# Performance work log

Hardware: AMD Instinct MI355X
Metric: run time of the kernel (lower is better)

## Reference

```python
import jax, jax.numpy as jnp
import numpy as np
from jax import lax

GN_EPS = 1e-5


def _conv2d(x, w, b, pad):
    # x: (N, C, H, W), w: (O, I, kh, kw)
    y = lax.conv_general_dilated(x, w, window_strides=(1, 1),
                                 padding=[(pad, pad), (pad, pad)],
                                 dimension_numbers=('NCHW', 'OIHW', 'NCHW'))
    return y + b[None, :, None, None]


def _eca(x, eca_w, eca_b):
    # x: (N, C, H, W) -> channel attention (N, C, 1, 1)
    y = jnp.mean(x, axis=(2, 3))[:, None, :]  # (N, 1, C) : GAP then treat C as length
    y = lax.conv_general_dilated(y, eca_w, window_strides=(1,),
                                 padding=[(1, 1)],
                                 dimension_numbers=('NCH', 'OIH', 'NCH'))
    y = jax.nn.sigmoid(y + eca_b[None, :, None])  # (N, 1, C)
    return y[:, 0, :, None, None]  # (N, C, 1, 1)


def _group_norm_per_channel(x, gn_w, gn_b):
    # num_groups == num_channels: normalize each channel over (H, W)
    mean = jnp.mean(x, axis=(2, 3), keepdims=True)
    var = jnp.var(x, axis=(2, 3), keepdims=True)
    xhat = (x - mean) * lax.rsqrt(var + GN_EPS)
    return xhat * gn_w[None, :, None, None] + gn_b[None, :, None, None]


def setup_inputs() -> dict:
    key = jax.random.key(0)
    ks = jax.random.split(key, 8)
    b, c, h, w = 16, 512, 64, 64
    cg = c // 32  # 16
    s = 1.0 / np.sqrt(cg)
    return {
        'x': jax.random.normal(ks[0], (b, c, h, w), jnp.float32),
        'conv1x1_w': jax.random.normal(ks[1], (cg, cg, 1, 1), jnp.float32) * s,
        'conv1x1_b': jnp.zeros((cg,), jnp.float32),
        'conv3x3_w': jax.random.normal(ks[2], (cg, cg, 3, 3), jnp.float32) * (s / 3),
        'conv3x3_b': jnp.zeros((cg,), jnp.float32),
        'conv5x5_w': jax.random.normal(ks[3], (cg, cg, 5, 5), jnp.float32) * (s / 5),
        'conv5x5_b': jnp.zeros((cg,), jnp.float32),
        'gn_w': jnp.ones((cg,), jnp.float32),
        'gn_b': jnp.zeros((cg,), jnp.float32),
        'eca_w': jax.random.normal(ks[4], (1, 1, 3), jnp.float32) * 0.5,
        'eca_b': jnp.zeros((1,), jnp.float32),
        'groups': 32,
    }


def reference(x, conv1x1_w, conv1x1_b, conv3x3_w, conv3x3_b,
              conv5x5_w, conv5x5_b, gn_w, gn_b, eca_w, eca_b, groups):
    b, c, h, w = x.shape
    cg = c // groups
    bg = b * groups
    group_x = x.reshape(bg, cg, h, w)

    # coordinate attention branch
    x_h = jnp.mean(group_x, axis=3, keepdims=True)            # (bg, cg, h, 1)
    x_w = jnp.mean(group_x, axis=2, keepdims=True)            # (bg, cg, 1, w)
    x_w_t = jnp.transpose(x_w, (0, 1, 3, 2))                  # (bg, cg, w, 1)
    hw = _conv2d(jnp.concatenate([x_h, x_w_t], axis=2), conv1x1_w, conv1x1_b, 0)
    x_h2, x_w2 = hw[:, :, :h, :], hw[:, :, h:, :]             # (bg,cg,h,1), (bg,cg,w,1)
    gated = group_x * jax.nn.sigmoid(x_h2) * jax.nn.sigmoid(jnp.transpose(x_w2, (0, 1, 3, 2)))
    x1 = _group_norm_per_channel(gated, gn_w, gn_b)

    # parallel conv branches
    x2 = _conv2d(group_x, conv3x3_w, conv3x3_b, 1)
    x3 = _conv2d(group_x, conv5x5_w, conv5x5_b, 2)

    # shared ECA channel attention over the three branches
    ca = _eca(x1, eca_w, eca_b) + _eca(x2, eca_w, eca_b) + _eca(x3, eca_w, eca_b)
    group_x = group_x * ca

    # cross-scale softmax-bmm interactions
    def chan_softmax(v):
        # (bg, cg, h, w) -> softmax over channel means -> (bg, 1, cg)
        return jax.nn.softmax(jnp.mean(v, axis=(2, 3)), axis=-1)[:, None, :]

    x11, x21, x31 = chan_softmax(x1), chan_softmax(x2), chan_softmax(x3)
    f1 = x1.reshape(bg, cg, h * w)
    f2 = x2.reshape(bg, cg, h * w)
    f3 = x3.reshape(bg, cg, h * w)

    weights = (jnp.matmul(x11, f2) + jnp.matmul(x11, f3)
               + jnp.matmul(x21, f1) + jnp.matmul(x21, f3)
               + jnp.matmul(x31, f1) + jnp.matmul(x31, f2))  # (bg, 1, h*w)
    weights = jax.nn.sigmoid(weights.reshape(bg, 1, h, w))

    return (group_x * weights).reshape(b, c, h, w)
```

## Files before the change

### kernel.cpp

```cpp
#include <hip/hip_runtime.h>

typedef unsigned int u32;

#define CG   16
#define HWN  4096
#define LSTR 68

__device__ __forceinline__ float sigm(float x) { return 1.0f / (1.0f + __expf(-x)); }

__global__ __launch_bounds__(512, 4) void ema_kernel(
    const float* __restrict__ x,
    const float* __restrict__ w1, const float* __restrict__ b1,
    const float* __restrict__ w3, const float* __restrict__ b3,
    const float* __restrict__ w5, const float* __restrict__ b5,
    const float* __restrict__ gnw, const float* __restrict__ gnb,
    const float* __restrict__ ew, const float* __restrict__ eb,
    float* __restrict__ out)
{
  __shared__ __align__(16) float s_cb[2][68][LSTR];
  __shared__ __align__(16) float s_row[16][64];
  __shared__ __align__(16) float s_col[16][64];
  __shared__ __align__(16) float s_RS[16][25];
  __shared__ float s_p2[16][16], s_p3[16][16];
  __shared__ __align__(16) float s_sh[16][64];
  __shared__ __align__(16) float s_sw[16][64];
  __shared__ __align__(16) float s_W5[16][28];
  __shared__ float s_ca[16], s_A1[16], s_Cc[16];
  __shared__ float s_w1[256], s_b1[16], s_gnw[16], s_gnb[16], s_b3[16], s_b5[16], s_ecaw[3], s_ecab[1];
  __shared__ float s_m2[16], s_m3[16], s_sm1[16], s_sm2[16], s_sm3[16];
  __shared__ float s_a1[16], s_a2[16], s_a3[16], s_total[16];
  __shared__ float s_red[16][8][2];
  __shared__ float s_scal[2];

  const int g = blockIdx.x;
  const int t = threadIdx.x;
  const int wv = t >> 6;
  const int ln = t & 63;
  const float* px   = x   + (size_t)g * CG * HWN;
  float*       pout = out + (size_t)g * CG * HWN;

  {
    const int j4 = ln & 15;
    const int rr = ln >> 4;
    #pragma unroll 1
    for (int cc = 0; cc < 2; ++cc) {
      const int c = 2 * wv + cc;
      float rs[16];
      float cp0 = 0.f, cp1 = 0.f, cp2 = 0.f, cp3 = 0.f;
      #pragma unroll
      for (int j = 0; j < 16; ++j) {
        float4 v = *(const float4*)(px + c * HWN + (rr + 4 * j) * 64 + 4 * j4);
        rs[j] = v.x + v.y + v.z + v.w;
        cp0 += v.x; cp1 += v.y; cp2 += v.z; cp3 += v.w;
      }
      #pragma unroll
      for (int j = 0; j < 16; ++j) {
        float r = rs[j];
        r += __shfl_xor(r, 1); r += __shfl_xor(r, 2);
        r += __shfl_xor(r, 4); r += __shfl_xor(r, 8);
        if (j4 == 0) s_row[c][rr + 4 * j] = r;
      }
      cp0 += __shfl_xor(cp0, 16); cp0 += __shfl_xor(cp0, 32);
      cp1 += __shfl_xor(cp1, 16); cp1 += __shfl_xor(cp1, 32);
      cp2 += __shfl_xor(cp2, 16); cp2 += __shfl_xor(cp2, 32);
      cp3 += __shfl_xor(cp3, 16); cp3 += __shfl_xor(cp3, 32);
      if (rr == 0) *(float4*)&s_col[c][4 * j4] = make_float4(cp0, cp1, cp2, cp3);
    }
  }
  if (t < 256) s_w1[t] = w1[t];
  if (t < 16) {
    s_b1[t]  = b1[t];  s_gnw[t] = gnw[t]; s_gnb[t] = gnb[t];
    s_b3[t]  = b3[t];  s_b5[t]  = b5[t];
  }
  if (t < 3)  s_ecaw[t] = ew[t];
  if (t == 0) s_ecab[0] = eb[0];
  __syncthreads();

  if (t < 16) { float s = 0.f; for (int y = 0; y < 64; ++y) s += s_row[t][y]; s_total[t] = s; }
  __syncthreads();

  #pragma unroll
  for (int m = 0; m < 4; ++m) {
    int idx = t + 512 * m; int o = idx >> 7, pos = idx & 127;
    float acc = s_b1[o];
    const float inv64 = 1.0f / 64.0f;
    #pragma unroll
    for (int i = 0; i < 16; ++i) {
      float v = (pos < 64 ? s_row[i][pos] : s_col[i][pos - 64]) * inv64;
      acc += s_w1[o * 16 + i] * v;
    }
    float sg = sigm(acc);
    if (pos < 64) s_sh[o][pos] = sg; else s_sw[o][pos - 64] = sg;
  }
  #pragma unroll
  for (int m = 0; m < 5; ++m) { int idx = t + 512 * m; if (idx < 2312) ((float4*)s_cb)[idx] = make_float4(0.f, 0.f, 0.f, 0.f); }
  if (t < 400) {
    int i = t / 25, kk = t % 25;
    int dy = kk / 5 - 2, dx = kk % 5 - 2;
    int a  = dy > 0 ? dy : 0,   b  = 64 + (dy < 0 ? dy : 0);
    int cl = dx > 0 ? dx : 0,   d  = 64 + (dx < 0 ? dx : 0);
    float S = s_total[i];
    if (a > 0)  S -= s_row[i][0];
    if (a > 1)  S -= s_row[i][1];
    if (b < 64) S -= s_row[i][63];
    if (b < 63) S -= s_row[i][62];
    for (int x0 = 0; x0 < cl; ++x0) {
      float cv = s_col[i][x0];
      if (a > 0)  cv -= px[i * HWN + 0 * 64  + x0];
      if (a > 1)  cv -= px[i * HWN + 1 * 64  + x0];
      if (b < 64) cv -= px[i * HWN + 63 * 64 + x0];
      if (b < 63) cv -= px[i * HWN + 62 * 64 + x0];
      S -= cv;
    }
    for (int x0 = d; x0 < 64; ++x0) {
      float cv = s_col[i][x0];
      if (a > 0)  cv -= px[i * HWN + 0 * 64  + x0];
      if (a > 1)  cv -= px[i * HWN + 1 * 64  + x0];
      if (b < 64) cv -= px[i * HWN + 63 * 64 + x0];
      if (b < 63) cv -= px[i * HWN + 62 * 64 + x0];
      S -= cv;
    }
    s_RS[i][kk] = S;
  }
  __syncthreads();

  if (t < 256) {
    int o = t >> 4, i = t & 15;
    float p2 = 0.f, p3 = 0.f;
    const float* w3b = w3 + (o * 16 + i) * 9;
    const float* w5b = w5 + (o * 16 + i) * 25;
    #pragma unroll
    for (int ky = 0; ky < 3; ++ky)
      #pragma unroll
      for (int kx = 0; kx < 3; ++kx)
        p2 += w3b[ky * 3 + kx] * s_RS[i][(ky + 1) * 5 + (kx + 1)];
    #pragma unroll
    for (int kk = 0; kk < 25; ++kk) p3 += w5b[kk] * s_RS[i][kk];
    s_p2[o][i] = p2; s_p3[o][i] = p3;
  }
  __syncthreads();
  if (t < 16)      { float s = 0.f; for (int i = 0; i < 16; ++i) s += s_p2[t][i];      s_m2[t] = s_b3[t] + s * (1.0f/4096.0f); }
  else if (t < 32) { int o = t - 16; float s = 0.f; for (int i = 0; i < 16; ++i) s += s_p3[o][i]; s_m3[o] = s_b5[o] + s * (1.0f/4096.0f); }
  __syncthreads();

  if (t < 3) {
    const float* m = (t == 0) ? s_gnb : (t == 1) ? s_m2 : s_m3;
    float* dst     = (t == 0) ? s_sm1 : (t == 1) ? s_sm2 : s_sm3;
    float mx = m[0];
    for (int c = 1; c < 16; ++c) mx = fmaxf(mx, m[c]);
    float e[16], ssum = 0.f;
    for (int c = 0; c < 16; ++c) { e[c] = __expf(m[c] - mx); ssum += e[c]; }
    float r = 1.0f / ssum;
    for (int c = 0; c < 16; ++c) dst[c] = e[c] * r;
  }
  __syncthreads();

  if (t < 16) {
    int c = t;
    float casum = 0.f;
    #pragma unroll
    for (int v = 0; v < 3; ++v) {
      const float* m = (v == 0) ? s_gnb : (v == 1) ? s_m2 : s_m3;
      float acc = s_ecab[0] + s_ecaw[1] * m[c];
      if (c > 0)  acc += s_ecaw[0] * m[c - 1];
      if (c < 15) acc += s_ecaw[2] * m[c + 1];
      casum += sigm(acc);
    }
    s_ca[c] = casum;
    s_a1[c] = s_sm2[c] + s_sm3[c];
    s_a2[c] = s_sm1[c] + s_sm3[c];
    s_a3[c] = s_sm1[c] + s_sm2[c];
  }
  __syncthreads();

  #define STAGE(buf, c) {                                                \
    _Pragma("unroll")                                                    \
    for (int k = 0; k < 2; ++k) {                                        \
      int q = t + 512 * k;                                               \
      int rr = q >> 4, xc = (q & 15) * 4;                                \
      float4 v = *(const float4*)(px + (size_t)(c) * HWN + rr * 64 + xc);\
      float* d = &s_cb[buf][2 + rr][2 + xc];                             \
      *(float2*)d       = make_float2(v.x, v.y);                         \
      *(float2*)(d + 2) = make_float2(v.z, v.w);                         \
    }                                                                    \
  }

  if (t == 0) {
    float s = 0.f;
    for (int o = 0; o < 16; ++o) s += s_a2[o] * s_b3[o] + s_a3[o] * s_b5[o];
    s_scal[1] = s;
  }
  if (t < 448) {
    if (t < 400) {
      int i = t / 25, kk = t % 25, ky = kk / 5, kx = kk % 5;
      float acc = 0.f;
      #pragma unroll
      for (int o = 0; o < 16; ++o) acc += s_a3[o] * w5[((o * 16 + i) * 5 + ky) * 5 + kx];
      if (ky >= 1 && ky <= 3 && kx >= 1 && kx <= 3) {
        #pragma unroll
        for (int o = 0; o < 16; ++o) acc += s_a2[o] * w3[((o * 16 + i) * 3 + (ky - 1)) * 3 + (kx - 1)];
      }
      s_W5[i][kk] = acc;
    } else {
      int q = t - 400; s_W5[q / 3][25 + q % 3] = 0.f;
    }
  }
  STAGE(0, 0);
  __syncthreads();

  const int x0 = 4 * (t & 15);
  const int y0 = 2 * (t >> 4);

  float ws[8];
  #pragma unroll
  for (int i = 0; i < 8; ++i) ws[i] = 0.f;
  float gsv[2][8];

  #pragma unroll 1
  for (int c = 0; c < 16; ++c) {
    if (c < 15) STAGE((c + 1) & 1, c + 1);
    if (c >= 1 && t == 0) {
      float S = 0.f, Q = 0.f;
      #pragma unroll
      for (int w = 0; w < 8; ++w) { S += s_red[c-1][w][0]; Q += s_red[c-1][w][1]; }
      float mu  = S * (1.0f / 4096.0f);
      float var = Q * (1.0f / 4096.0f) - mu * mu;
      float inv = rsqrtf(var + 1e-5f);
      s_A1[c-1] = s_a1[c-1] * s_gnw[c-1] * inv;
      s_Cc[c-1] = s_a1[c-1] * (s_gnb[c-1] - mu * s_gnw[c-1] * inv);
    }
    if (c >= 2) {
      float a1v = s_A1[c-2];
      #pragma unroll
      for (int i = 0; i < 8; ++i) ws[i] += a1v * gsv[c & 1][i];
    }
    float Wk[28];
    #pragma unroll
    for (int i = 0; i < 7; ++i) *(float4*)&Wk[4 * i] = *(float4*)&s_W5[c][4 * i];
    float shv0 = s_sh[c][y0], shv1 = s_sh[c][y0 + 1];
    float swv[4];
    #pragma unroll
    for (int r = 0; r < 4; ++r) swv[r] = s_sw[c][x0 + r];
    const float* base = &s_cb[c & 1][0][0] + y0 * LSTR + x0;
    float gsl = 0.f, gql = 0.f;
    #pragma unroll
    for (int q = 0; q < 6; ++q) {
      const float* rp = base + q * LSTR;
      float4 A = *(const float4*)rp, B = *(const float4*)(rp + 4);
      float v[8] = {A.x, A.y, A.z, A.w, B.x, B.y, B.z, B.w};
      if (q == 2 || q == 3) {
        const float sh_ = (q == 2) ? shv0 : shv1;
        const int ri = q - 2;
        #pragma unroll
        for (int m = 0; m < 4; ++m) {
          float gg = v[m + 2] * sh_ * swv[m];
          gsl += gg; gql += gg * gg;
          gsv[c & 1][4 * ri + m] = gg;
        }
      }
      #pragma unroll
      for (int r = 0; r < 2; ++r) {
        const int kr = q - r;
        if (kr >= 0 && kr <= 4) {
          #pragma unroll
          for (int m = 0; m < 4; ++m) {
            float a = ws[4 * r + m];
            a += Wk[kr * 5 + 0] * v[m + 0];
            a += Wk[kr * 5 + 1] * v[m + 1];
            a += Wk[kr * 5 + 2] * v[m + 2];
            a += Wk[kr * 5 + 3] * v[m + 3];
            a += Wk[kr * 5 + 4] * v[m + 4];
            ws[4 * r + m] = a;
          }
        }
      }
    }
    gsl += __shfl_xor(gsl, 1);  gql += __shfl_xor(gql, 1);
    gsl += __shfl_xor(gsl, 2);  gql += __shfl_xor(gql, 2);
    gsl += __shfl_xor(gsl, 4);  gql += __shfl_xor(gql, 4);
    gsl += __shfl_xor(gsl, 8);  gql += __shfl_xor(gql, 8);
    gsl += __shfl_xor(gsl, 16); gql += __shfl_xor(gql, 16);
    gsl += __shfl_xor(gsl, 32); gql += __shfl_xor(gql, 32);
    if (ln == 0) { s_red[c][wv][0] = gsl; s_red[c][wv][1] = gql; }
    __syncthreads();
  }

  if (t == 0) {
    float S = 0.f, Q = 0.f;
    #pragma unroll
    for (int w = 0; w < 8; ++w) { S += s_red[15][w][0]; Q += s_red[15][w][1]; }
    float mu  = S * (1.0f / 4096.0f);
    float var = Q * (1.0f / 4096.0f) - mu * mu;
    float inv = rsqrtf(var + 1e-5f);
    s_A1[15] = s_a1[15] * s_gnw[15] * inv;
    s_Cc[15] = s_a1[15] * (s_gnb[15] - mu * s_gnw[15] * inv);
    float s = s_scal[1];
    for (int c = 0; c < 16; ++c) s += s_Cc[c];
    s_scal[0] = s;
  }
  __syncthreads();
  {
    const float a14 = s_A1[14], a15 = s_A1[15], Ct = s_scal[0];
    #pragma unroll
    for (int i = 0; i < 8; ++i)
      ws[i] = sigm(ws[i] + a14 * gsv[0][i] + a15 * gsv[1][i] + Ct);
  }

  #pragma unroll
  for (int c = 0; c < 16; ++c) {
    const float cav = s_ca[c];
    const float* xp = px   + c * HWN + y0 * 64 + x0;
    float*       op = pout + c * HWN + y0 * 64 + x0;
    float4 xa = *(const float4*)xp;
    float4 xb = *(const float4*)(xp + 64);
    float4 oa, ob;
    oa.x = xa.x * cav * ws[0]; oa.y = xa.y * cav * ws[1];
    oa.z = xa.z * cav * ws[2]; oa.w = xa.w * cav * ws[3];
    ob.x = xb.x * cav * ws[4]; ob.y = xb.y * cav * ws[5];
    ob.z = xb.z * cav * ws[6]; ob.w = xb.w * cav * ws[7];
    *(float4*)op        = oa;
    *(float4*)(op + 64) = ob;
  }
}

extern "C" void kernel_launch(void* const* d_in, const int* in_sizes, int n_in,
                              void* d_out, int out_size, void* d_ws, size_t ws_size,
                              hipStream_t stream) {
  const float* X  = (const float*)d_in[0];
  const float* W1 = (const float*)d_in[1];
  const float* B1 = (const float*)d_in[2];
  const float* W3 = (const float*)d_in[3];
  const float* B3 = (const float*)d_in[4];
  const float* W5 = (const float*)d_in[5];
  const float* B5 = (const float*)d_in[6];
  const float* GW = (const float*)d_in[7];
  const float* GB = (const float*)d_in[8];
  const float* EW = (const float*)d_in[9];
  const float* EB = (const float*)d_in[10];
  float* O = (float*)d_out;
  ema_kernel<<<dim3(512), dim3(512), 0, stream>>>(X, W1, B1, W3, B3, W5, B5, GW, GB, EW, EB, O);
}
```

Measured before the change: 345.1 us.

## Alias scratch arrays into conv staging buffer, split staging load/write, nontemporal stores

Reuses the second half of the double-buffered conv tile for the row/col sums, RS and partial-product scratch, cutting LDS per block, and raises the launch-bounds occupancy hint from 4 to 6 blocks per CU. Staging of the next channel is split into a global load issued at the top of the loop and an LDS write after the conv compute, so the load latency is hidden behind the arithmetic. Output stores become nontemporal. The split keeps extra live registers across the loop, which together with the tighter launch bound risks spills.

```diff
diff --git a/kernel.cpp b/kernel.cpp
--- a/kernel.cpp
+++ b/kernel.cpp
@@ -1,6 +1,7 @@
 #include <hip/hip_runtime.h>
 
 typedef unsigned int u32;
+typedef float f4v __attribute__((ext_vector_type(4)));
 
 #define CG   16
 #define HWN  4096
@@ -8,7 +9,7 @@
 
 __device__ __forceinline__ float sigm(float x) { return 1.0f / (1.0f + __expf(-x)); }
 
-__global__ __launch_bounds__(512, 4) void ema_kernel(
+__global__ __launch_bounds__(512, 6) void ema_kernel(
     const float* __restrict__ x,
     const float* __restrict__ w1, const float* __restrict__ b1,
     const float* __restrict__ w3, const float* __restrict__ b3,
@@ -18,10 +19,11 @@
     float* __restrict__ out)
 {
   __shared__ __align__(16) float s_cb[2][68][LSTR];
-  __shared__ __align__(16) float s_row[16][64];
-  __shared__ __align__(16) float s_col[16][64];
-  __shared__ __align__(16) float s_RS[16][25];
-  __shared__ float s_p2[16][16], s_p3[16][16];
+  float* const s_row = &s_cb[1][0][0];
+  float* const s_col = s_row + 1024;
+  float* const s_RS  = s_row + 2048;
+  float* const s_p2  = s_row + 2448;
+  float* const s_p3  = s_row + 2704;
   __shared__ __align__(16) float s_sh[16][64];
   __shared__ __align__(16) float s_sw[16][64];
   __shared__ __align__(16) float s_W5[16][28];
@@ -58,13 +60,13 @@
         float r = rs[j];
         r += __shfl_xor(r, 1); r += __shfl_xor(r, 2);
         r += __shfl_xor(r, 4); r += __shfl_xor(r, 8);
-        if (j4 == 0) s_row[c][rr + 4 * j] = r;
+        if (j4 == 0) s_row[c * 64 + rr + 4 * j] = r;
       }
       cp0 += __shfl_xor(cp0, 16); cp0 += __shfl_xor(cp0, 32);
       cp1 += __shfl_xor(cp1, 16); cp1 += __shfl_xor(cp1, 32);
       cp2 += __shfl_xor(cp2, 16); cp2 += __shfl_xor(cp2, 32);
       cp3 += __shfl_xor(cp3, 16); cp3 += __shfl_xor(cp3, 32);
-      if (rr == 0) *(float4*)&s_col[c][4 * j4] = make_float4(cp0, cp1, cp2, cp3);
+      if (rr == 0) *(float4*)&s_col[c * 64 + 4 * j4] = make_float4(cp0, cp1, cp2, cp3);
     }
   }
   if (t < 256) s_w1[t] = w1[t];
@@ -76,7 +78,7 @@
   if (t == 0) s_ecab[0] = eb[0];
   __syncthreads();
 
-  if (t < 16) { float s = 0.f; for (int y = 0; y < 64; ++y) s += s_row[t][y]; s_total[t] = s; }
+  if (t < 16) { float s = 0.f; for (int y = 0; y < 64; ++y) s += s_row[t * 64 + y]; s_total[t] = s; }
   __syncthreads();
 
   #pragma unroll
@@ -86,26 +88,26 @@
     const float inv64 = 1.0f / 64.0f;
     #pragma unroll
     for (int i = 0; i < 16; ++i) {
-      float v = (pos < 64 ? s_row[i][pos] : s_col[i][pos - 64]) * inv64;
+      float v = (pos < 64 ? s_row[i * 64 + pos] : s_col[i * 64 + pos - 64]) * inv64;
       acc += s_w1[o * 16 + i] * v;
     }
     float sg = sigm(acc);
     if (pos < 64) s_sh[o][pos] = sg; else s_sw[o][pos - 64] = sg;
   }
   #pragma unroll
-  for (int m = 0; m < 5; ++m) { int idx = t + 512 * m; if (idx < 2312) ((float4*)s_cb)[idx] = make_float4(0.f, 0.f, 0.f, 0.f); }
+  for (int m = 0; m < 3; ++m) { int idx = t + 512 * m; if (idx < 1156) ((float4*)&s_cb[0][0][0])[idx] = make_float4(0.f, 0.f, 0.f, 0.f); }
   if (t < 400) {
     int i = t / 25, kk = t % 25;
     int dy = kk / 5 - 2, dx = kk % 5 - 2;
     int a  = dy > 0 ? dy : 0,   b  = 64 + (dy < 0 ? dy : 0);
     int cl = dx > 0 ? dx : 0,   d  = 64 + (dx < 0 ? dx : 0);
     float S = s_total[i];
-    if (a > 0)  S -= s_row[i][0];
-    if (a > 1)  S -= s_row[i][1];
-    if (b < 64) S -= s_row[i][63];
-    if (b < 63) S -= s_row[i][62];
+    if (a > 0)  S -= s_row[i * 64 + 0];
+    if (a > 1)  S -= s_row[i * 64 + 1];
+    if (b < 64) S -= s_row[i * 64 + 63];
+    if (b < 63) S -= s_row[i * 64 + 62];
     for (int x0 = 0; x0 < cl; ++x0) {
-      float cv = s_col[i][x0];
+      float cv = s_col[i * 64 + x0];
       if (a > 0)  cv -= px[i * HWN + 0 * 64  + x0];
       if (a > 1)  cv -= px[i * HWN + 1 * 64  + x0];
       if (b < 64) cv -= px[i * HWN + 63 * 64 + x0];
@@ -113,14 +115,14 @@
       S -= cv;
     }
     for (int x0 = d; x0 < 64; ++x0) {
-      float cv = s_col[i][x0];
+      float cv = s_col[i * 64 + x0];
       if (a > 0)  cv -= px[i * HWN + 0 * 64  + x0];
       if (a > 1)  cv -= px[i * HWN + 1 * 64  + x0];
       if (b < 64) cv -= px[i * HWN + 63 * 64 + x0];
       if (b < 63) cv -= px[i * HWN + 62 * 64 + x0];
       S -= cv;
     }
-    s_RS[i][kk] = S;
+    s_RS[i * 25 + kk] = S;
   }
   __syncthreads();
 
@@ -133,16 +135,18 @@
     for (int ky = 0; ky < 3; ++ky)
       #pragma unroll
       for (int kx = 0; kx < 3; ++kx)
-        p2 += w3b[ky * 3 + kx] * s_RS[i][(ky + 1) * 5 + (kx + 1)];
-    #pragma unroll
-    for (int kk = 0; kk < 25; ++kk) p3 += w5b[kk] * s_RS[i][kk];
-    s_p2[o][i] = p2; s_p3[o][i] = p3;
-  }
-  __syncthreads();
-  if (t < 16)      { float s = 0.f; for (int i = 0; i < 16; ++i) s += s_p2[t][i];      s_m2[t] = s_b3[t] + s * (1.0f/4096.0f); }
-  else if (t < 32) { int o = t - 16; float s = 0.f; for (int i = 0; i < 16; ++i) s += s_p3[o][i]; s_m3[o] = s_b5[o] + s * (1.0f/4096.0f); }
-  __syncthreads();
-
+        p2 += w3b[ky * 3 + kx] * s_RS[i * 25 + (ky + 1) * 5 + (kx + 1)];
+    #pragma unroll
+    for (int kk = 0; kk < 25; ++kk) p3 += w5b[kk] * s_RS[i * 25 + kk];
+    s_p2[o * 16 + i] = p2; s_p3[o * 16 + i] = p3;
+  }
+  __syncthreads();
+  if (t < 16)      { float s = 0.f; for (int i = 0; i < 16; ++i) s += s_p2[t * 16 + i];        s_m2[t] = s_b3[t] + s * (1.0f/4096.0f); }
+  else if (t < 32) { int o = t - 16; float s = 0.f; for (int i = 0; i < 16; ++i) s += s_p3[o * 16 + i]; s_m3[o] = s_b5[o] + s * (1.0f/4096.0f); }
+  __syncthreads();
+
+  #pragma unroll
+  for (int m = 0; m < 3; ++m) { int idx = t + 512 * m; if (idx < 1156) ((float4*)&s_cb[1][0][0])[idx] = make_float4(0.f, 0.f, 0.f, 0.f); }
   if (t < 3) {
     const float* m = (t == 0) ? s_gnb : (t == 1) ? s_m2 : s_m3;
     float* dst     = (t == 0) ? s_sm1 : (t == 1) ? s_sm2 : s_sm3;
@@ -173,16 +177,18 @@
   }
   __syncthreads();
 
-  #define STAGE(buf, c) {                                                \
-    _Pragma("unroll")                                                    \
-    for (int k = 0; k < 2; ++k) {                                        \
-      int q = t + 512 * k;                                               \
-      int rr = q >> 4, xc = (q & 15) * 4;                                \
-      float4 v = *(const float4*)(px + (size_t)(c) * HWN + rr * 64 + xc);\
-      float* d = &s_cb[buf][2 + rr][2 + xc];                             \
-      *(float2*)d       = make_float2(v.x, v.y);                         \
-      *(float2*)(d + 2) = make_float2(v.z, v.w);                         \
-    }                                                                    \
+  #define STAGE_LOAD(c, ra, rb) {                                        \
+    const float* sp = px + (size_t)(c) * HWN + (t >> 4) * 64 + (t & 15) * 4; \
+    ra = *(const float4*)sp;                                             \
+    rb = *(const float4*)(sp + 2048);                                    \
+  }
+  #define STAGE_WRITE(buf, ra, rb) {                                     \
+    float* d0 = &s_cb[buf][2 + (t >> 4)][2 + (t & 15) * 4];              \
+    *(float2*)d0       = make_float2(ra.x, ra.y);                        \
+    *(float2*)(d0 + 2) = make_float2(ra.z, ra.w);                        \
+    float* d1 = d0 + 32 * LSTR;                                          \
+    *(float2*)d1       = make_float2(rb.x, rb.y);                        \
+    *(float2*)(d1 + 2) = make_float2(rb.z, rb.w);                        \
   }
 
   if (t == 0) {
@@ -205,7 +211,11 @@
       int q = t - 400; s_W5[q / 3][25 + q % 3] = 0.f;
     }
   }
-  STAGE(0, 0);
+  {
+    float4 p0, p1;
+    STAGE_LOAD(0, p0, p1);
+    STAGE_WRITE(0, p0, p1);
+  }
   __syncthreads();
 
   const int x0 = 4 * (t & 15);
@@ -215,10 +225,11 @@
   #pragma unroll
   for (int i = 0; i < 8; ++i) ws[i] = 0.f;
   float gsv[2][8];
+  float4 st0, st1;
 
   #pragma unroll 1
   for (int c = 0; c < 16; ++c) {
-    if (c < 15) STAGE((c + 1) & 1, c + 1);
+    if (c < 15) STAGE_LOAD(c + 1, st0, st1);
     if (c >= 1 && t == 0) {
       float S = 0.f, Q = 0.f;
       #pragma unroll
@@ -275,6 +286,7 @@
         }
       }
     }
+    if (c < 15) STAGE_WRITE((c + 1) & 1, st0, st1);
     gsl += __shfl_xor(gsl, 1);  gql += __shfl_xor(gql, 1);
     gsl += __shfl_xor(gsl, 2);  gql += __shfl_xor(gql, 2);
     gsl += __shfl_xor(gsl, 4);  gql += __shfl_xor(gql, 4);
@@ -318,8 +330,8 @@
     oa.z = xa.z * cav * ws[2]; oa.w = xa.w * cav * ws[3];
     ob.x = xb.x * cav * ws[4]; ob.y = xb.y * cav * ws[5];
     ob.z = xb.z * cav * ws[6]; ob.w = xb.w * cav * ws[7];
-    *(float4*)op        = oa;
-    *(float4*)(op + 64) = ob;
+    __builtin_nontemporal_store(*(f4v*)&oa, (f4v*)op);
+    __builtin_nontemporal_store(*(f4v*)&ob, (f4v*)(op + 64));
   }
 }
 
```

Result: slower. 692.0 us (+100.5%).

## Split EMA into prep kernel and band-parallel main kernel via global params

Applied to the files above, without the earlier changes.

The single fused kernel becomes two. A prep kernel computes per-group statistics, the group-norm coefficients (now taken from an extra pass over x in place of the streaming reduction) and the folded conv weights, then writes them to a global parameter buffer. A main kernel launches four times as many blocks, each handling a 16-row band with halo, to raise parallelism and occupancy and drop the serialized per-channel reduction. The cost is an extra launch, extra reads of x in prep and halo rows, and a global round trip for the parameters.

```diff
diff --git a/kernel.cpp b/kernel.cpp
--- a/kernel.cpp
+++ b/kernel.cpp
@@ -1,43 +1,39 @@
 #include <hip/hip_runtime.h>
-
-typedef unsigned int u32;
 
 #define CG   16
 #define HWN  4096
 #define LSTR 68
+#define PSTRIDE 2560
+
+__device__ float g_params[512 * PSTRIDE];
 
 __device__ __forceinline__ float sigm(float x) { return 1.0f / (1.0f + __expf(-x)); }
 
-__global__ __launch_bounds__(512, 4) void ema_kernel(
+__global__ __launch_bounds__(512, 4) void ema_prep(
     const float* __restrict__ x,
     const float* __restrict__ w1, const float* __restrict__ b1,
     const float* __restrict__ w3, const float* __restrict__ b3,
     const float* __restrict__ w5, const float* __restrict__ b5,
     const float* __restrict__ gnw, const float* __restrict__ gnb,
-    const float* __restrict__ ew, const float* __restrict__ eb,
-    float* __restrict__ out)
+    const float* __restrict__ ew, const float* __restrict__ eb)
 {
-  __shared__ __align__(16) float s_cb[2][68][LSTR];
-  __shared__ __align__(16) float s_row[16][64];
-  __shared__ __align__(16) float s_col[16][64];
-  __shared__ __align__(16) float s_RS[16][25];
+  __shared__ float s_row[16][64], s_col[16][64];
+  __shared__ float s_RS[16][25];
   __shared__ float s_p2[16][16], s_p3[16][16];
   __shared__ __align__(16) float s_sh[16][64];
   __shared__ __align__(16) float s_sw[16][64];
   __shared__ __align__(16) float s_W5[16][28];
-  __shared__ float s_ca[16], s_A1[16], s_Cc[16];
   __shared__ float s_w1[256], s_b1[16], s_gnw[16], s_gnb[16], s_b3[16], s_b5[16], s_ecaw[3], s_ecab[1];
   __shared__ float s_m2[16], s_m3[16], s_sm1[16], s_sm2[16], s_sm3[16];
-  __shared__ float s_a1[16], s_a2[16], s_a3[16], s_total[16];
-  __shared__ float s_red[16][8][2];
+  __shared__ float s_a1[16], s_a2[16], s_a3[16], s_total[16], s_ca[16];
+  __shared__ float s_A1[16], s_Cc[16];
   __shared__ float s_scal[2];
 
   const int g = blockIdx.x;
   const int t = threadIdx.x;
   const int wv = t >> 6;
   const int ln = t & 63;
-  const float* px   = x   + (size_t)g * CG * HWN;
-  float*       pout = out + (size_t)g * CG * HWN;
+  const float* px = x + (size_t)g * CG * HWN;
 
   {
     const int j4 = ln & 15;
@@ -92,8 +88,6 @@
     float sg = sigm(acc);
     if (pos < 64) s_sh[o][pos] = sg; else s_sw[o][pos - 64] = sg;
   }
-  #pragma unroll
-  for (int m = 0; m < 5; ++m) { int idx = t + 512 * m; if (idx < 2312) ((float4*)s_cb)[idx] = make_float4(0.f, 0.f, 0.f, 0.f); }
   if (t < 400) {
     int i = t / 25, kk = t % 25;
     int dy = kk / 5 - 2, dx = kk % 5 - 2;
@@ -173,18 +167,6 @@
   }
   __syncthreads();
 
-  #define STAGE(buf, c) {                                                \
-    _Pragma("unroll")                                                    \
-    for (int k = 0; k < 2; ++k) {                                        \
-      int q = t + 512 * k;                                               \
-      int rr = q >> 4, xc = (q & 15) * 4;                                \
-      float4 v = *(const float4*)(px + (size_t)(c) * HWN + rr * 64 + xc);\
-      float* d = &s_cb[buf][2 + rr][2 + xc];                             \
-      *(float2*)d       = make_float2(v.x, v.y);                         \
-      *(float2*)(d + 2) = make_float2(v.z, v.w);                         \
-    }                                                                    \
-  }
-
   if (t == 0) {
     float s = 0.f;
     for (int o = 0; o < 16; ++o) s += s_a2[o] * s_b3[o] + s_a3[o] * s_b5[o];
@@ -205,121 +187,148 @@
       int q = t - 400; s_W5[q / 3][25 + q % 3] = 0.f;
     }
   }
-  STAGE(0, 0);
-  __syncthreads();
-
-  const int x0 = 4 * (t & 15);
-  const int y0 = 2 * (t >> 4);
-
-  float ws[8];
-  #pragma unroll
-  for (int i = 0; i < 8; ++i) ws[i] = 0.f;
-  float gsv[2][8];
-
-  #pragma unroll 1
-  for (int c = 0; c < 16; ++c) {
-    if (c < 15) STAGE((c + 1) & 1, c + 1);
-    if (c >= 1 && t == 0) {
-      float S = 0.f, Q = 0.f;
-      #pragma unroll
-      for (int w = 0; w < 8; ++w) { S += s_red[c-1][w][0]; Q += s_red[c-1][w][1]; }
-      float mu  = S * (1.0f / 4096.0f);
-      float var = Q * (1.0f / 4096.0f) - mu * mu;
-      float inv = rsqrtf(var + 1e-5f);
-      s_A1[c-1] = s_a1[c-1] * s_gnw[c-1] * inv;
-      s_Cc[c-1] = s_a1[c-1] * (s_gnb[c-1] - mu * s_gnw[c-1] * inv);
-    }
-    if (c >= 2) {
-      float a1v = s_A1[c-2];
-      #pragma unroll
-      for (int i = 0; i < 8; ++i) ws[i] += a1v * gsv[c & 1][i];
-    }
-    float Wk[28];
-    #pragma unroll
-    for (int i = 0; i < 7; ++i) *(float4*)&Wk[4 * i] = *(float4*)&s_W5[c][4 * i];
-    float shv0 = s_sh[c][y0], shv1 = s_sh[c][y0 + 1];
-    float swv[4];
-    #pragma unroll
-    for (int r = 0; r < 4; ++r) swv[r] = s_sw[c][x0 + r];
-    const float* base = &s_cb[c & 1][0][0] + y0 * LSTR + x0;
-    float gsl = 0.f, gql = 0.f;
-    #pragma unroll
-    for (int q = 0; q < 6; ++q) {
-      const float* rp = base + q * LSTR;
-      float4 A = *(const float4*)rp, B = *(const float4*)(rp + 4);
-      float v[8] = {A.x, A.y, A.z, A.w, B.x, B.y, B.z, B.w};
-      if (q == 2 || q == 3) {
-        const float sh_ = (q == 2) ? shv0 : shv1;
-        const int ri = q - 2;
-        #pragma unroll
-        for (int m = 0; m < 4; ++m) {
-          float gg = v[m + 2] * sh_ * swv[m];
-          gsl += gg; gql += gg * gg;
-          gsv[c & 1][4 * ri + m] = gg;
-        }
-      }
-      #pragma unroll
-      for (int r = 0; r < 2; ++r) {
-        const int kr = q - r;
-        if (kr >= 0 && kr <= 4) {
-          #pragma unroll
-          for (int m = 0; m < 4; ++m) {
-            float a = ws[4 * r + m];
-            a += Wk[kr * 5 + 0] * v[m + 0];
-            a += Wk[kr * 5 + 1] * v[m + 1];
-            a += Wk[kr * 5 + 2] * v[m + 2];
-            a += Wk[kr * 5 + 3] * v[m + 3];
-            a += Wk[kr * 5 + 4] * v[m + 4];
-            ws[4 * r + m] = a;
-          }
-        }
-      }
-    }
-    gsl += __shfl_xor(gsl, 1);  gql += __shfl_xor(gql, 1);
-    gsl += __shfl_xor(gsl, 2);  gql += __shfl_xor(gql, 2);
-    gsl += __shfl_xor(gsl, 4);  gql += __shfl_xor(gql, 4);
-    gsl += __shfl_xor(gsl, 8);  gql += __shfl_xor(gql, 8);
-    gsl += __shfl_xor(gsl, 16); gql += __shfl_xor(gql, 16);
-    gsl += __shfl_xor(gsl, 32); gql += __shfl_xor(gql, 32);
-    if (ln == 0) { s_red[c][wv][0] = gsl; s_red[c][wv][1] = gql; }
-    __syncthreads();
-  }
-
+
+  {
+    const int j4 = ln & 15;
+    const int rr = ln >> 4;
+    #pragma unroll 1
+    for (int cc = 0; cc < 2; ++cc) {
+      const int c = 2 * wv + cc;
+      float gs = 0.f, gq = 0.f;
+      const float4 swq = *(const float4*)&s_sw[c][4 * j4];
+      #pragma unroll
+      for (int j = 0; j < 16; ++j) {
+        const int y = rr + 4 * j;
+        float4 v = *(const float4*)(px + c * HWN + y * 64 + 4 * j4);
+        const float shv = s_sh[c][y];
+        float g0 = v.x * shv * swq.x, g1 = v.y * shv * swq.y;
+        float g2 = v.z * shv * swq.z, g3 = v.w * shv * swq.w;
+        gs += (g0 + g1) + (g2 + g3);
+        gq += (g0 * g0 + g1 * g1) + (g2 * g2 + g3 * g3);
+      }
+      gs += __shfl_xor(gs, 1);  gq += __shfl_xor(gq, 1);
+      gs += __shfl_xor(gs, 2);  gq += __shfl_xor(gq, 2);
+      gs += __shfl_xor(gs, 4);  gq += __shfl_xor(gq, 4);
+      gs += __shfl_xor(gs, 8);  gq += __shfl_xor(gq, 8);
+      gs += __shfl_xor(gs, 16); gq += __shfl_xor(gq, 16);
+      gs += __shfl_xor(gs, 32); gq += __shfl_xor(gq, 32);
+      if (ln == 0) {
+        float mu  = gs * (1.0f / 4096.0f);
+        float var = gq * (1.0f / 4096.0f) - mu * mu;
+        float inv = rsqrtf(var + 1e-5f);
+        s_A1[c] = s_a1[c] * s_gnw[c] * inv;
+        s_Cc[c] = s_a1[c] * (s_gnb[c] - mu * s_gnw[c] * inv);
+      }
+    }
+  }
+  __syncthreads();
   if (t == 0) {
-    float S = 0.f, Q = 0.f;
-    #pragma unroll
-    for (int w = 0; w < 8; ++w) { S += s_red[15][w][0]; Q += s_red[15][w][1]; }
-    float mu  = S * (1.0f / 4096.0f);
-    float var = Q * (1.0f / 4096.0f) - mu * mu;
-    float inv = rsqrtf(var + 1e-5f);
-    s_A1[15] = s_a1[15] * s_gnw[15] * inv;
-    s_Cc[15] = s_a1[15] * (s_gnb[15] - mu * s_gnw[15] * inv);
     float s = s_scal[1];
     for (int c = 0; c < 16; ++c) s += s_Cc[c];
     s_scal[0] = s;
   }
   __syncthreads();
-  {
-    const float a14 = s_A1[14], a15 = s_A1[15], Ct = s_scal[0];
-    #pragma unroll
-    for (int i = 0; i < 8; ++i)
-      ws[i] = sigm(ws[i] + a14 * gsv[0][i] + a15 * gsv[1][i] + Ct);
-  }
-
+
+  float* wp = g_params + (size_t)g * PSTRIDE;
+  for (int i = t; i < 1024; i += 512) wp[i]        = s_sh[i >> 6][i & 63];
+  for (int i = t; i < 1024; i += 512) wp[1024 + i] = s_sw[i >> 6][i & 63];
+  if (t < 448) wp[2048 + t] = s_W5[t / 28][t % 28];
+  if (t < 16) { wp[2496 + t] = s_A1[t]; wp[2512 + t] = s_ca[t]; }
+  if (t == 0) wp[2528] = s_scal[0];
+}
+
+__global__ __launch_bounds__(256, 6) void ema_main(
+    const float* __restrict__ x, float* __restrict__ out)
+{
+  __shared__ __align__(16) float s_t[2][20][LSTR];
+  __shared__ float m_sh[16][16];
+  __shared__ __align__(16) float m_sw[16][64];
+  __shared__ __align__(16) float m_W5[16][28];
+  __shared__ float m_A1[16], m_ca[16], m_Ct[1];
+
+  const int bid  = blockIdx.x;
+  const int g    = bid >> 2;
+  const int band = bid & 3;
+  const int r0   = band * 16;
+  const int t    = threadIdx.x;
+  const float* px   = x   + (size_t)g * CG * HWN;
+  float*       pout = out + (size_t)g * CG * HWN;
+  const float* wp = g_params + (size_t)g * PSTRIDE;
+
+  if (t < 256) m_sh[t >> 4][t & 15] = wp[(t >> 4) * 64 + r0 + (t & 15)];
+  for (int i = t; i < 1024; i += 256) m_sw[i >> 6][i & 63] = wp[1024 + i];
+  for (int i = t; i < 448; i += 256)  m_W5[i / 28][i % 28] = wp[2048 + i];
+  if (t < 16) { m_A1[t] = wp[2496 + t]; m_ca[t] = wp[2512 + t]; }
+  if (t == 0) m_Ct[0] = wp[2528];
+  for (int i = t; i < 2 * 20 * LSTR / 2; i += 256) ((float2*)s_t)[i] = make_float2(0.f, 0.f);
+  __syncthreads();
+
+  const int srow = t >> 4, sc4 = t & 15;
+  #define MSTAGE(buf, c) {                                                     \
+    { int i = srow, y = r0 - 2 + i;                                            \
+      if ((unsigned)y < 64u) {                                                 \
+        float4 v = *(const float4*)(px + (size_t)(c) * HWN + y * 64 + 4 * sc4);\
+        float* d = &s_t[buf][i][2 + 4 * sc4];                                  \
+        *(float2*)d       = make_float2(v.x, v.y);                             \
+        *(float2*)(d + 2) = make_float2(v.z, v.w); } }                         \
+    if (t < 64) { int i = 16 + srow, y = r0 - 2 + i;                           \
+      if ((unsigned)y < 64u) {                                                 \
+        float4 v = *(const float4*)(px + (size_t)(c) * HWN + y * 64 + 4 * sc4);\
+        float* d = &s_t[buf][i][2 + 4 * sc4];                                  \
+        *(float2*)d       = make_float2(v.x, v.y);                             \
+        *(float2*)(d + 2) = make_float2(v.z, v.w); } }                         \
+  }
+
+  MSTAGE(0, 0);
+  __syncthreads();
+
+  const int tx = t & 15, ty = t >> 4;
+  const int x0 = 4 * tx;
+  float ws0 = 0.f, ws1 = 0.f, ws2 = 0.f, ws3 = 0.f;
+
+  #pragma unroll 1
+  for (int c = 0; c < 16; ++c) {
+    if (c < 15) MSTAGE((c + 1) & 1, c + 1);
+    const int buf = c & 1;
+    const float shv = m_sh[c][ty];
+    const float sw0 = m_sw[c][x0],     sw1 = m_sw[c][x0 + 1];
+    const float sw2 = m_sw[c][x0 + 2], sw3 = m_sw[c][x0 + 3];
+    const float a1v = m_A1[c];
+    #pragma unroll
+    for (int k = 0; k < 5; ++k) {
+      const float* rp = &s_t[buf][ty + k][x0];
+      float4 A = *(const float4*)rp, B = *(const float4*)(rp + 4);
+      const float v0 = A.x, v1 = A.y, v2 = A.z, v3 = A.w;
+      const float v4 = B.x, v5 = B.y, v6 = B.z, v7 = B.w;
+      const float Wa = m_W5[c][5 * k],     Wb = m_W5[c][5 * k + 1];
+      const float Wc = m_W5[c][5 * k + 2], Wd = m_W5[c][5 * k + 3];
+      const float We = m_W5[c][5 * k + 4];
+      ws0 += Wa * v0 + Wb * v1 + Wc * v2 + Wd * v3 + We * v4;
+      ws1 += Wa * v1 + Wb * v2 + Wc * v3 + Wd * v4 + We * v5;
+      ws2 += Wa * v2 + Wb * v3 + Wc * v4 + Wd * v5 + We * v6;
+      ws3 += Wa * v3 + Wb * v4 + Wc * v5 + Wd * v6 + We * v7;
+      if (k == 2) {
+        ws0 += a1v * (v2 * shv * sw0);
+        ws1 += a1v * (v3 * shv * sw1);
+        ws2 += a1v * (v4 * shv * sw2);
+        ws3 += a1v * (v5 * shv * sw3);
+      }
+    }
+    __syncthreads();
+  }
+
+  const float Ct = m_Ct[0];
+  const float f0 = sigm(ws0 + Ct), f1 = sigm(ws1 + Ct);
+  const float f2 = sigm(ws2 + Ct), f3 = sigm(ws3 + Ct);
+  const int rowoff = (r0 + ty) * 64 + x0;
   #pragma unroll
   for (int c = 0; c < 16; ++c) {
-    const float cav = s_ca[c];
-    const float* xp = px   + c * HWN + y0 * 64 + x0;
-    float*       op = pout + c * HWN + y0 * 64 + x0;
-    float4 xa = *(const float4*)xp;
-    float4 xb = *(const float4*)(xp + 64);
-    float4 oa, ob;
-    oa.x = xa.x * cav * ws[0]; oa.y = xa.y * cav * ws[1];
-    oa.z = xa.z * cav * ws[2]; oa.w = xa.w * cav * ws[3];
-    ob.x = xb.x * cav * ws[4]; ob.y = xb.y * cav * ws[5];
-    ob.z = xb.z * cav * ws[6]; ob.w = xb.w * cav * ws[7];
-    *(float4*)op        = oa;
-    *(float4*)(op + 64) = ob;
+    const float cav = m_ca[c];
+    float4 xv = *(const float4*)(px + c * HWN + rowoff);
+    float4 o;
+    o.x = xv.x * cav * f0; o.y = xv.y * cav * f1;
+    o.z = xv.z * cav * f2; o.w = xv.w * cav * f3;
+    *(float4*)(pout + c * HWN + rowoff) = o;
   }
 }
 
@@ -338,5 +347,6 @@
   const float* EW = (const float*)d_in[9];
   const float* EB = (const float*)d_in[10];
   float* O = (float*)d_out;
-  ema_kernel<<<dim3(512), dim3(512), 0, stream>>>(X, W1, B1, W3, B3, W5, B5, GW, GB, EW, EB, O);
+  ema_prep<<<dim3(512), dim3(512), 0, stream>>>(X, W1, B1, W3, B3, W5, B5, GW, GB, EW, EB);
+  ema_main<<<dim3(2048), dim3(256), 0, stream>>>(X, O);
 }
```

Measured after the change: 345.0 us. Within noise of the previous version (-0.0%).
